# Optimization experiments

Measured on AMD Instinct MI355X. Metric: run time of the kernel, lower is better.

The kernel has to match this reference:

```python
import jax, jax.numpy as jnp
import numpy as np

WS = 15
PAD = WS // 2
BN_EPS = 1e-5


def _unfold2d(a, ws):
    # a: (b, t, c, H, W) already padded -> (b, t, c, h, w, ws, ws), stride-1 windows
    h = a.shape[3] - ws + 1
    w = a.shape[4] - ws + 1
    ih = (jnp.arange(h)[:, None] + jnp.arange(ws)[None, :])  # (h, ws)
    iw = (jnp.arange(w)[:, None] + jnp.arange(ws)[None, :])  # (w, ws)
    return a[:, :, :, ih[:, None, :, None], iw[None, :, None, :]]


def setup_inputs() -> dict:
    key = jax.random.key(0)
    ks = jax.random.split(key, 11)
    b, t_mem, c, h, w = 2, 2, 256, 32, 32
    s = 0.05
    return {
        "x": jax.random.normal(ks[0], (b, c, h, w), jnp.float32),
        "mem": jax.random.normal(ks[1], (b, t_mem, c, h, w), jnp.float32),
        "w_qk": jax.random.normal(ks[2], (c // 8, c), jnp.float32) * s,
        "w_qv": jax.random.normal(ks[3], (c // 2, c), jnp.float32) * s,
        "w_mk": jax.random.normal(ks[4], (c // 8, c), jnp.float32) * s,
        "w_mv": jax.random.normal(ks[5], (c // 2, c), jnp.float32) * s,
        "w_smooth": jax.random.normal(ks[6], (c, c), jnp.float32) * s,
        "bn_gamma": jax.random.uniform(ks[7], (c,), jnp.float32, 0.5, 1.5),
        "bn_beta": jax.random.normal(ks[8], (c,), jnp.float32) * 0.1,
        "bn_mean": jnp.zeros((c,), jnp.float32),
        "bn_var": jnp.ones((c,), jnp.float32),
    }


def reference(x, mem, w_qk, w_qv, w_mk, w_mv, w_smooth, bn_gamma, bn_beta, bn_mean, bn_var):
    # mem <- cat([x, mem]) along time: (b, t, c, h, w)
    mem = jnp.concatenate([x[:, None], mem], axis=1)
    b, t, c, h, w = mem.shape

    # 1x1 convs == per-pixel matmuls
    query_k = jnp.einsum('bchw,oc->bohw', x, w_qk)          # (b, c/8, h, w)
    query_v = jnp.einsum('bchw,oc->bohw', x, w_qv)          # (b, c/2, h, w); Dropout2d(p=0) is identity
    mem_k = jnp.einsum('btchw,oc->btohw', mem, w_mk)        # (b, t, c/8, h, w)
    mem_v = jnp.einsum('btchw,oc->btohw', mem, w_mv)        # (b, t, c/2, h, w)

    pad = [(0, 0), (0, 0), (0, 0), (PAD, PAD), (PAD, PAD)]
    unf_k = _unfold2d(jnp.pad(mem_k, pad), WS)              # (b, t, c/8, h, w, ws, ws)
    unf_v = _unfold2d(jnp.pad(mem_v, pad), WS)              # (b, t, c/2, h, w, ws, ws)

    attn = jnp.einsum('bchw,btchwxy->bhwtxy', query_k, unf_k)
    attn = attn.reshape(b, h, w, t * WS * WS)
    # NOTE: faithful to original: softmax over dim=2 (the spatial w axis), not over keys
    attn = jax.nn.softmax(attn, axis=2)

    unf_v = jnp.transpose(unf_v, (0, 2, 3, 4, 1, 5, 6)).reshape(b, c // 2, h, w, t * WS * WS)
    mem_out = jnp.einsum('bhwk,bchwk->bchw', attn, unf_v)   # (b, c/2, h, w)

    feat = jnp.concatenate([query_v, mem_out], axis=1)      # (b, c, h, w)
    y = jnp.einsum('bchw,oc->bohw', feat, w_smooth)
    # BatchNorm2d in eval mode (running stats) + ReLU
    inv = bn_gamma / jnp.sqrt(bn_var + BN_EPS)
    y = y * inv[None, :, None, None] + (bn_beta - bn_mean * inv)[None, :, None, None]
    return jax.nn.relu(y)
```

## Files before the change

### kernel.cpp

```cpp
#include <hip/hip_runtime.h>
#include <math.h>

#define HWSZ 1024
#define HH 32
#define WW 32
#define C 256
#define CK 32
#define CV 128
#define T 3
#define WSZ 15
#define PADSZ 7
#define PADDED 46
#define PP (PADDED*PADDED)
#define KK (T*WSZ*WSZ)
#define B 2
#define NOUT 160
#define KC 32
#define PIXT 32

static const size_t OFF_QK   = 0;
static const size_t OFF_QV   = 65536;
static const size_t OFF_MK   = 327680;
static const size_t OFF_MV   = 733952;
static const size_t OFF_PART = 2359040;

__global__ __launch_bounds__(256) void k_proj(
    const float* __restrict__ x, const float* __restrict__ mem,
    const float* __restrict__ w_qk, const float* __restrict__ w_qv,
    const float* __restrict__ w_mk, const float* __restrict__ w_mv,
    float* __restrict__ ws)
{
    __shared__ float inT[KC][PIXT];
    __shared__ float wT[NOUT][KC + 1];

    int jb   = blockIdx.x >> 5;
    int rowt = blockIdx.x & 31;
    int tid  = threadIdx.x;
    int tx   = tid & 7;
    int ty   = tid >> 3;

    int b, t;
    const float *wk, *wv;
    bool isq;
    if (jb < 6) { b = jb / 3; t = jb % 3; wk = w_mk; wv = w_mv; isq = false; }
    else        { b = jb - 6; t = 0;      wk = w_qk; wv = w_qv; isq = true;  }

    const float* src = (t == 0)
        ? (x + ((size_t)b * C) * HWSZ)
        : (mem + ((size_t)(b * (T - 1) + (t - 1)) * C) * HWSZ);
    int hw0 = rowt * WW;

    float* mk = ws + OFF_MK;
    float* mv = ws + OFF_MV;
    size_t bt = (size_t)(b * T + t);

    if (!isq) {
        int yp = rowt + PADSZ;
        for (int f = tid; f < 448 + 1792; f += 256) {
            if (f < 448) {
                int c = f >> 4, sc = f & 15;
                if (sc < 14) {
                    int col = (sc < 7) ? sc : sc + 25;
                    mk[(bt * PP + yp * PADDED + col) * CK + c] = 0.f;
                }
            } else {
                int g = f - 448;
                int sc = g >> 7, c = g & 127;
                int col = (sc < 7) ? sc : sc + 25;
                mv[(bt * PP + yp * PADDED + col) * CV + c] = 0.f;
            }
        }
        if (rowt < 14) {
            int pr = (rowt < 7) ? rowt : rowt + 32;
            for (int f = tid; f < 1472 + 5888; f += 256) {
                if (f < 1472) {
                    int col = f >> 5, c = f & 31;
                    mk[(bt * PP + pr * PADDED + col) * CK + c] = 0.f;
                } else {
                    int g = f - 1472;
                    int col = g >> 7, c = g & 127;
                    mv[(bt * PP + pr * PADDED + col) * CV + c] = 0.f;
                }
            }
        }
    }

    float acc[5][4];
    #pragma unroll
    for (int j = 0; j < 5; j++)
        #pragma unroll
        for (int i = 0; i < 4; i++) acc[j][i] = 0.f;

    for (int c0 = 0; c0 < C; c0 += KC) {
        {
            int cc = tid >> 3;
            int p4 = (tid & 7) * 4;
            float4 v = *(const float4*)&src[(size_t)(c0 + cc) * HWSZ + hw0 + p4];
            inT[cc][p4 + 0] = v.x; inT[cc][p4 + 1] = v.y;
            inT[cc][p4 + 2] = v.z; inT[cc][p4 + 3] = v.w;
        }
        #pragma unroll
        for (int j = 0; j < 5; j++) {
            int f  = tid + j * 256;
            int o  = f >> 3;
            int c4 = (f & 7) * 4;
            const float* wr = (o < CK) ? (wk + (size_t)o * C) : (wv + (size_t)(o - CK) * C);
            float4 v = *(const float4*)&wr[c0 + c4];
            wT[o][c4 + 0] = v.x; wT[o][c4 + 1] = v.y;
            wT[o][c4 + 2] = v.z; wT[o][c4 + 3] = v.w;
        }
        __syncthreads();

        #pragma unroll 8
        for (int k = 0; k < KC; k++) {
            float4 iv = *(const float4*)&inT[k][tx * 4];
            #pragma unroll
            for (int j = 0; j < 5; j++) {
                float wv_ = wT[ty * 5 + j][k];
                acc[j][0] += wv_ * iv.x; acc[j][1] += wv_ * iv.y;
                acc[j][2] += wv_ * iv.z; acc[j][3] += wv_ * iv.w;
            }
        }
        __syncthreads();
    }

    int hq = rowt, yp = hq + PADSZ;
    #pragma unroll
    for (int j = 0; j < 5; j++) {
        int o = ty * 5 + j;
        #pragma unroll
        for (int i = 0; i < 4; i++) {
            int wq = tx * 4 + i;
            float v = acc[j][i];
            if (!isq) {
                int xp = wq + PADSZ;
                if (o < CK)
                    mk[(bt * PP + yp * PADDED + xp) * CK + o] = v;
                else
                    mv[(bt * PP + yp * PADDED + xp) * CV + (o - CK)] = v;
            } else {
                int hw = hq * WW + wq;
                if (o < CK) ws[OFF_QK + ((size_t)b * HWSZ + hw) * CK + o] = v;
                else        ws[OFF_QV + ((size_t)(b * CV + (o - CK))) * HWSZ + hw] = v;
            }
        }
    }
}

__global__ __launch_bounds__(256) void k_attn_av(
    const float* __restrict__ qk, const float* __restrict__ mk,
    const float* __restrict__ mv, float* __restrict__ part)
{
    __shared__ float al[2][WSZ][WW];

    int blk = blockIdx.x;
    int xg  = blk % 3;
    int rem = blk / 3;
    int t   = rem % T;
    int bh  = rem / T;
    int b   = bh >> 5, hq = bh & 31;
    int tid = threadIdx.x;

    const float* mkb = mk + (size_t)(b * T + t) * PP * CK;
    const float* mvb = mv + (size_t)(b * T + t) * PP * CV;

    int w  = tid & 31;
    int ty = tid >> 5;

    float4 q[8];
    {
        const float* qrow = qk + ((size_t)(b * HWSZ + hq * WW + w)) * CK;
        #pragma unroll
        for (int i = 0; i < 8; i++) q[i] = *(const float4*)&qrow[i * 4];
    }

    int c0 = w * 4;
    int w0 = ty * 4;

    float acc[4][4];
    #pragma unroll
    for (int ci = 0; ci < 4; ci++)
        #pragma unroll
        for (int wi = 0; wi < 4; wi++) acc[ci][wi] = 0.f;

    int yy0 = ty, yy1r = (ty + 8 < WSZ) ? ty + 8 : WSZ - 1;
    bool has1 = (ty + 8 < WSZ);

    for (int xi = 0; xi < 5; xi++) {
        int xx = xg * 5 + xi;
        int buf = xi & 1;
        const float* mkrow = mkb + (size_t)(hq + xx) * PADDED * CK;
        const float* vrow  = mvb + (size_t)(hq + xx) * PADDED * CV + c0;

        float s0 = 0.f, s1 = 0.f;
        {
            const float* k0 = mkrow + (size_t)(w + yy0) * CK;
            const float* k1 = mkrow + (size_t)(w + yy1r) * CK;
            #pragma unroll
            for (int cq = 0; cq < 8; cq++) {
                float4 m0 = *(const float4*)&k0[cq * 4];
                float4 m1 = *(const float4*)&k1[cq * 4];
                s0 += q[cq].x * m0.x + q[cq].y * m0.y + q[cq].z * m0.z + q[cq].w * m0.w;
                s1 += q[cq].x * m1.x + q[cq].y * m1.y + q[cq].z * m1.z + q[cq].w * m1.w;
            }
        }

        float4 vw[18];
        #pragma unroll
        for (int i = 0; i < 18; i++)
            vw[i] = *(const float4*)&vrow[(size_t)(w0 + i) * CV];

        {
            float m0 = s0, m1 = s1;
            #pragma unroll
            for (int d = 1; d < 32; d <<= 1) {
                m0 = fmaxf(m0, __shfl_xor(m0, d, 32));
                m1 = fmaxf(m1, __shfl_xor(m1, d, 32));
            }
            float e0 = __expf(s0 - m0), e1 = __expf(s1 - m1);
            float t0 = e0, t1 = e1;
            #pragma unroll
            for (int d = 1; d < 32; d <<= 1) {
                t0 += __shfl_xor(t0, d, 32);
                t1 += __shfl_xor(t1, d, 32);
            }
            al[buf][yy0][w] = e0 / t0;
            if (has1) al[buf][yy1r][w] = e1 / t1;
        }
        __syncthreads();

        #pragma unroll
        for (int yy = 0; yy < WSZ; yy++) {
            float4 a4 = *(const float4*)&al[buf][yy][w0];
            #pragma unroll
            for (int wi = 0; wi < 4; wi++) {
                float av = (wi == 0) ? a4.x : (wi == 1) ? a4.y : (wi == 2) ? a4.z : a4.w;
                float4 vv = vw[yy + wi];
                acc[0][wi] += av * vv.x;
                acc[1][wi] += av * vv.y;
                acc[2][wi] += av * vv.z;
                acc[3][wi] += av * vv.w;
            }
        }
    }

    float* pbase = part + ((size_t)(bh * 9 + (t * 3 + xg)) * CV) * WW;
    #pragma unroll
    for (int ci = 0; ci < 4; ci++) {
        float4 r; r.x = acc[ci][0]; r.y = acc[ci][1]; r.z = acc[ci][2]; r.w = acc[ci][3];
        *(float4*)&pbase[(c0 + ci) * WW + w0] = r;
    }
}

__global__ __launch_bounds__(256) void k_out(
    const float* __restrict__ qv, const float* __restrict__ part,
    const float* __restrict__ wsm,
    const float* __restrict__ g, const float* __restrict__ bta,
    const float* __restrict__ mean, const float* __restrict__ var,
    float* __restrict__ out)
{
    __shared__ float inT[KC][PIXT];
    __shared__ float wTt[KC][132];

    int blk  = blockIdx.x;
    int oh   = blk & 1;
    int rowt = (blk >> 1) & 31;
    int b    = blk >> 6;
    int tid  = threadIdx.x;
    int tx   = tid & 7;
    int ty   = tid >> 3;
    int hw0  = rowt * WW;
    int obase = oh * 128;
    int bh   = b * HH + rowt;

    float acc[4][4];
    #pragma unroll
    for (int j = 0; j < 4; j++)
        #pragma unroll
        for (int i = 0; i < 4; i++) acc[j][i] = 0.f;

    for (int c0 = 0; c0 < C; c0 += KC) {
        {
            int cc = tid >> 3;
            int p4 = (tid & 7) * 4;
            float4 v;
            if (c0 < CV) {
                v = *(const float4*)&qv[((size_t)(b * CV + c0 + cc)) * HWSZ + hw0 + p4];
            } else {
                int cloc = (c0 - CV) + cc;
                const float* pb = part + ((size_t)bh * 9) * CV * WW + cloc * WW + p4;
                float4 s = *(const float4*)pb;
                #pragma unroll
                for (int tg = 1; tg < 9; tg++) {
                    float4 a = *(const float4*)&pb[(size_t)tg * CV * WW];
                    s.x += a.x; s.y += a.y; s.z += a.z; s.w += a.w;
                }
                v = s;
            }
            inT[cc][p4 + 0] = v.x; inT[cc][p4 + 1] = v.y;
            inT[cc][p4 + 2] = v.z; inT[cc][p4 + 3] = v.w;
        }
        #pragma unroll
        for (int j = 0; j < 4; j++) {
            int f  = tid + j * 256;
            int o  = f >> 3;
            int c4 = (f & 7) * 4;
            float4 v = *(const float4*)&wsm[(size_t)(obase + o) * C + c0 + c4];
            wTt[c4 + 0][o] = v.x; wTt[c4 + 1][o] = v.y;
            wTt[c4 + 2][o] = v.z; wTt[c4 + 3][o] = v.w;
        }
        __syncthreads();

        #pragma unroll 8
        for (int k = 0; k < KC; k++) {
            float4 iv  = *(const float4*)&inT[k][tx * 4];
            float4 wv4 = *(const float4*)&wTt[k][ty * 4];
            acc[0][0] += wv4.x * iv.x; acc[0][1] += wv4.x * iv.y;
            acc[0][2] += wv4.x * iv.z; acc[0][3] += wv4.x * iv.w;
            acc[1][0] += wv4.y * iv.x; acc[1][1] += wv4.y * iv.y;
            acc[1][2] += wv4.y * iv.z; acc[1][3] += wv4.y * iv.w;
            acc[2][0] += wv4.z * iv.x; acc[2][1] += wv4.z * iv.y;
            acc[2][2] += wv4.z * iv.z; acc[2][3] += wv4.z * iv.w;
            acc[3][0] += wv4.w * iv.x; acc[3][1] += wv4.w * iv.y;
            acc[3][2] += wv4.w * iv.z; acc[3][3] += wv4.w * iv.w;
        }
        __syncthreads();
    }

    #pragma unroll
    for (int j = 0; j < 4; j++) {
        int o = obase + ty * 4 + j;
        float inv = g[o] * rsqrtf(var[o] + 1e-5f);
        float sh  = bta[o] - mean[o] * inv;
        float4 r;
        r.x = fmaxf(acc[j][0] * inv + sh, 0.f);
        r.y = fmaxf(acc[j][1] * inv + sh, 0.f);
        r.z = fmaxf(acc[j][2] * inv + sh, 0.f);
        r.w = fmaxf(acc[j][3] * inv + sh, 0.f);
        *(float4*)&out[((size_t)(b * C + o)) * HWSZ + hw0 + tx * 4] = r;
    }
}

extern "C" void kernel_launch(void* const* d_in, const int* in_sizes, int n_in,
                              void* d_out, int out_size, void* d_ws, size_t ws_size,
                              hipStream_t stream) {
    const float* x    = (const float*)d_in[0];
    const float* mem  = (const float*)d_in[1];
    const float* w_qk = (const float*)d_in[2];
    const float* w_qv = (const float*)d_in[3];
    const float* w_mk = (const float*)d_in[4];
    const float* w_mv = (const float*)d_in[5];
    const float* wsm  = (const float*)d_in[6];
    const float* g    = (const float*)d_in[7];
    const float* bta  = (const float*)d_in[8];
    const float* mean = (const float*)d_in[9];
    const float* var  = (const float*)d_in[10];
    float* out = (float*)d_out;
    float* ws  = (float*)d_ws;

    k_proj<<<8 * 32, 256, 0, stream>>>(x, mem, w_qk, w_qv, w_mk, w_mv, ws);
    k_attn_av<<<B * HH * T * 3, 256, 0, stream>>>(ws + OFF_QK, ws + OFF_MK,
                                                  ws + OFF_MV, ws + OFF_PART);
    k_out<<<B * 32 * 2, 256, 0, stream>>>(ws + OFF_QV, ws + OFF_PART, wsm,
                                          g, bta, mean, var, out);
}
```

Before: 94.45 us.

## Split attention value channels across two blocks and remap block indices per XCD

```diff
diff --git a/kernel.cpp b/kernel.cpp
--- a/kernel.cpp
+++ b/kernel.cpp
@@ -154,10 +154,12 @@
     __shared__ float al[2][WSZ][WW];
 
     int blk = blockIdx.x;
-    int xg  = blk % 3;
-    int rem = blk / 3;
-    int t   = rem % T;
-    int bh  = rem / T;
+    int xcd = blk & 7;
+    int loc = blk >> 3;
+    int ch  = loc & 1;  loc >>= 1;
+    int xg  = loc % 3;  loc /= 3;
+    int t   = loc % 3;
+    int bh  = xcd * 8 + loc / 3;
     int b   = bh >> 5, hq = bh & 31;
     int tid = threadIdx.x;
 
@@ -174,17 +176,28 @@
         for (int i = 0; i < 8; i++) q[i] = *(const float4*)&qrow[i * 4];
     }
 
-    int c0 = w * 4;
-    int w0 = ty * 4;
-
-    float acc[4][4];
-    #pragma unroll
-    for (int ci = 0; ci < 4; ci++)
+    int cq = tid & 31;
+    int wg = tid >> 5;
+    int c0 = ch * 64 + cq * 2;
+    int w0 = wg * 4;
+
+    float acc[2][4];
+    #pragma unroll
+    for (int ci = 0; ci < 2; ci++)
         #pragma unroll
         for (int wi = 0; wi < 4; wi++) acc[ci][wi] = 0.f;
 
     int yy0 = ty, yy1r = (ty + 8 < WSZ) ? ty + 8 : WSZ - 1;
     bool has1 = (ty + 8 < WSZ);
+
+    for (int xi = 0; xi < 3; xi++) {
+        int xx = xg * 5 + xi;
+        xx = xg + xi * 3;
+        xx = xg * 3 + xi;
+        (void)xx;
+        int dummy = 0; (void)dummy;
+        break;
+    }
 
     for (int xi = 0; xi < 5; xi++) {
         int xx = xg * 5 + xi;
@@ -197,18 +210,18 @@
             const float* k0 = mkrow + (size_t)(w + yy0) * CK;
             const float* k1 = mkrow + (size_t)(w + yy1r) * CK;
             #pragma unroll
-            for (int cq = 0; cq < 8; cq++) {
-                float4 m0 = *(const float4*)&k0[cq * 4];
-                float4 m1 = *(const float4*)&k1[cq * 4];
-                s0 += q[cq].x * m0.x + q[cq].y * m0.y + q[cq].z * m0.z + q[cq].w * m0.w;
-                s1 += q[cq].x * m1.x + q[cq].y * m1.y + q[cq].z * m1.z + q[cq].w * m1.w;
-            }
-        }
-
-        float4 vw[18];
+            for (int cc = 0; cc < 8; cc++) {
+                float4 m0 = *(const float4*)&k0[cc * 4];
+                float4 m1 = *(const float4*)&k1[cc * 4];
+                s0 += q[cc].x * m0.x + q[cc].y * m0.y + q[cc].z * m0.z + q[cc].w * m0.w;
+                s1 += q[cc].x * m1.x + q[cc].y * m1.y + q[cc].z * m1.z + q[cc].w * m1.w;
+            }
+        }
+
+        float2 vw[18];
         #pragma unroll
         for (int i = 0; i < 18; i++)
-            vw[i] = *(const float4*)&vrow[(size_t)(w0 + i) * CV];
+            vw[i] = *(const float2*)&vrow[(size_t)(w0 + i) * CV];
 
         {
             float m0 = s0, m1 = s1;
@@ -235,18 +248,16 @@
             #pragma unroll
             for (int wi = 0; wi < 4; wi++) {
                 float av = (wi == 0) ? a4.x : (wi == 1) ? a4.y : (wi == 2) ? a4.z : a4.w;
-                float4 vv = vw[yy + wi];
+                float2 vv = vw[yy + wi];
                 acc[0][wi] += av * vv.x;
                 acc[1][wi] += av * vv.y;
-                acc[2][wi] += av * vv.z;
-                acc[3][wi] += av * vv.w;
             }
         }
     }
 
     float* pbase = part + ((size_t)(bh * 9 + (t * 3 + xg)) * CV) * WW;
     #pragma unroll
-    for (int ci = 0; ci < 4; ci++) {
+    for (int ci = 0; ci < 2; ci++) {
         float4 r; r.x = acc[ci][0]; r.y = acc[ci][1]; r.z = acc[ci][2]; r.w = acc[ci][3];
         *(float4*)&pbase[(c0 + ci) * WW + w0] = r;
     }
@@ -359,8 +370,8 @@
     float* ws  = (float*)d_ws;
 
     k_proj<<<8 * 32, 256, 0, stream>>>(x, mem, w_qk, w_qv, w_mk, w_mv, ws);
-    k_attn_av<<<B * HH * T * 3, 256, 0, stream>>>(ws + OFF_QK, ws + OFF_MK,
-                                                  ws + OFF_MV, ws + OFF_PART);
+    k_attn_av<<<B * HH * T * 3 * 2, 256, 0, stream>>>(ws + OFF_QK, ws + OFF_MK,
+                                                      ws + OFF_MV, ws + OFF_PART);
     k_out<<<B * 32 * 2, 256, 0, stream>>>(ws + OFF_QV, ws + OFF_PART, wsm,
                                           g, bta, mean, var, out);
 }
```

After: 126.9 us. 1.34x slower.
